# Performance work log

Hardware: AMD Instinct MI355X
Metric: run time of the kernel (lower is better)

Reference implementation:

```python
import jax, jax.numpy as jnp
import numpy as np

B, T, FEAT, IN = 32, 96, 2048, 4096  # batch, frames, feature_len, inshape (cat mode)


def setup_inputs() -> dict:
    key = jax.random.key(0)
    ks = jax.random.split(key, 12)
    s = 1.0 / np.sqrt(FEAT)  # PyTorch LSTMCell/Linear init scale ~ U(-1/sqrt(hidden), ...)
    f32 = jnp.float32
    return {
        "feature": jax.random.normal(ks[0], (B, T, IN), f32),
        "gumbel_u": jax.random.uniform(ks[1], (T - 1, B, 2), f32),
        "W_ih": jax.random.normal(ks[2], (4 * FEAT, IN), f32) * s,
        "b_ih": jax.random.normal(ks[3], (4 * FEAT,), f32) * s,
        "W_hh": jax.random.normal(ks[4], (4 * FEAT, FEAT), f32) * s,
        "b_hh": jax.random.normal(ks[5], (4 * FEAT,), f32) * s,
        "W_pred": jax.random.normal(ks[6], (2, FEAT), f32) * s,
        "b_pred": jax.random.normal(ks[7], (2,), f32) * s,
        "W_util": jax.random.normal(ks[8], (1, FEAT), f32) * s,
        "b_util": jax.random.normal(ks[9], (1,), f32) * s,
        "W_use": jax.random.normal(ks[10], (2, FEAT), f32) * s,
        "b_use": jax.random.normal(ks[11], (2,), f32) * s,
    }


def reference(feature, gumbel_u, W_ih, b_ih, W_hh, b_hh,
              W_pred, b_pred, W_util, b_util, W_use, b_use):
    tau = 1.0
    eps = 1e-10
    x = jnp.transpose(feature, (1, 0, 2))          # [T, B, IN]
    gnoise = -jnp.log(-jnp.log(gumbel_u + eps) + eps)  # Gumbel(0,1), [T-1, B, 2]

    def lstm_cell(x_t, h, c):
        gates = x_t @ W_ih.T + b_ih + h @ W_hh.T + b_hh  # [B, 4F]
        i, f, g, o = jnp.split(gates, 4, axis=-1)        # PyTorch gate order i,f,g,o
        c2 = jax.nn.sigmoid(f) * c + jax.nn.sigmoid(i) * jnp.tanh(g)
        h2 = jax.nn.sigmoid(o) * jnp.tanh(c2)
        return h2, c2

    def heads(h):
        return h @ W_pred.T + b_pred, h @ W_util.T + b_util

    h0 = jnp.zeros((x.shape[1], FEAT), x.dtype)
    h, c = lstm_cell(x[0], h0, h0)                   # step 0: no gating
    pred0, util0 = heads(h)

    def step(carry, inp):
        h_prev, c_prev = carry
        x_t, g_t = inp
        h_new, c2 = lstm_cell(x_t, h_prev, c_prev)
        logits = h_new @ W_use.T + b_use             # [B, 2]
        use = jax.nn.softmax((logits + g_t) / tau, axis=-1)  # soft gumbel-softmax
        # bmm(stack([h_prev, h_new], -1), use) == convex mix of the two states
        h2 = h_prev * use[:, :1] + h_new * use[:, 1:2]
        pred, util = heads(h2)
        return (h2, c2), (pred, util)

    _, (preds, utils) = jax.lax.scan(step, (h, c), (x[1:], gnoise))
    pred = jnp.concatenate([pred0[None], preds], axis=0)   # [T, B, 2]
    util = jnp.concatenate([util0[None], utils], axis=0)   # [T, B, 1]
    return pred, util
```

## Files before the change

kernel.cpp:

```cpp
#include <hip/hip_runtime.h>
#include <cstdint>
#include <cstddef>

#define TT 96
#define BB 32
#define FEATD 2048
#define IND 4096
#define NG 8192
#define MROWS 3072

typedef _Float16 half8 __attribute__((ext_vector_type(8)));
typedef _Float16 half4 __attribute__((ext_vector_type(4)));
typedef float f32x4 __attribute__((ext_vector_type(4)));

#define WS_FEAT16 0u
#define WS_HBUF   0u
#define WS_WIH16  25165824u
#define WS_WHH16  92274688u
#define WS_PRE16  125829120u
#define WS_GAB    176160768u
#define WS_HD     176185344u
#define WS_BAR    176222208u

#define NWG 256
#define BAR_WORDS (33 * 64)

__global__ void __launch_bounds__(256) k_convert(
    const float* __restrict__ feat, const float* __restrict__ wih,
    const float* __restrict__ whh,
    _Float16* __restrict__ feat16, _Float16* __restrict__ wih16,
    _Float16* __restrict__ whh16, unsigned* __restrict__ barr)
{
  size_t id = (size_t)blockIdx.x * blockDim.x + threadIdx.x;
  size_t stride = (size_t)gridDim.x * blockDim.x;
  for (size_t i = id; i < (size_t)MROWS * IND / 4; i += stride) {
    f32x4 v = ((const f32x4*)feat)[i];
    half4 h = { (_Float16)v[0], (_Float16)v[1], (_Float16)v[2], (_Float16)v[3] };
    ((half4*)feat16)[i] = h;
  }
  for (size_t i = id; i < (size_t)NG * IND / 4; i += stride) {
    f32x4 v = ((const f32x4*)wih)[i];
    half4 h = { (_Float16)v[0], (_Float16)v[1], (_Float16)v[2], (_Float16)v[3] };
    ((half4*)wih16)[i] = h;
  }
  for (size_t i = id; i < (size_t)NG * FEATD / 4; i += stride) {
    f32x4 v = ((const f32x4*)whh)[i];
    half4 h = { (_Float16)v[0], (_Float16)v[1], (_Float16)v[2], (_Float16)v[3] };
    ((half4*)whh16)[i] = h;
  }
  for (size_t i = id; i < BAR_WORDS; i += stride) barr[i] = 0u;
}

__device__ __forceinline__ void gload16(const _Float16* g, _Float16* l) {
  __builtin_amdgcn_global_load_lds(
      (const __attribute__((address_space(1))) void*)g,
      (__attribute__((address_space(3))) void*)l, 16, 0, 0);
}

__global__ void __launch_bounds__(256, 1) k_gemm(
    const _Float16* __restrict__ A,
    const _Float16* __restrict__ Bw,
    const float* __restrict__ bih, const float* __restrict__ bhh,
    _Float16* __restrict__ C)
{
  __shared__ __align__(16) _Float16 As[128 * 32];
  __shared__ __align__(16) _Float16 Bs[128 * 32];
  const int tid = threadIdx.x;
  const int lane = tid & 63;
  const int wave = tid >> 6;
  const int wm = wave >> 1, wn = wave & 1;
  const int mbase = blockIdx.y * 128;
  const int nbase = blockIdx.x * 128;

  f32x4 acc[4][4] = {};
  const int r0 = lane >> 2;
  const int kc = (lane & 3) * 8;
  const int rr = lane & 15;
  const int ko = (lane >> 4) * 8;

  for (int k0 = 0; k0 < IND; k0 += 32) {
    for (int i = 0; i < 2; ++i) {
      int seg = wave * 2 + i;
      int row = seg * 16 + r0;
      gload16(A + (size_t)(mbase + row) * IND + k0 + kc, As + seg * 512);
      gload16(Bw + (size_t)(nbase + row) * IND + k0 + kc, Bs + seg * 512);
    }
    __syncthreads();
    half8 af[4], bf[4];
    for (int f = 0; f < 4; ++f) {
      af[f] = *(const half8*)(As + (wm * 64 + f * 16 + rr) * 32 + ko);
      bf[f] = *(const half8*)(Bs + (wn * 64 + f * 16 + rr) * 32 + ko);
    }
    for (int fm = 0; fm < 4; ++fm)
      for (int fn = 0; fn < 4; ++fn)
        acc[fm][fn] = __builtin_amdgcn_mfma_f32_16x16x32_f16(af[fm], bf[fn], acc[fm][fn], 0, 0, 0);
    __syncthreads();
  }
  for (int fn = 0; fn < 4; ++fn) {
    int n = nbase + wn * 64 + fn * 16 + (lane & 15);
    float bias = bih[n] + bhh[n];
    for (int fm = 0; fm < 4; ++fm) {
      int m0 = mbase + wm * 64 + fm * 16 + (lane >> 4) * 4;
      for (int r = 0; r < 4; ++r)
        C[(size_t)(m0 + r) * NG + n] = (_Float16)(acc[fm][fn][r] + bias);
    }
  }
}

#define LDS_WHH 0
#define LDS_RED 131072
#define RED_STRIDE_F 1152
#define LDS_G   149504
#define LDS_C   153728
#define LDS_TOTAL 154752

__global__ void __launch_bounds__(512, 1) k_recur(
    const float* __restrict__ gumbel,
    const float* __restrict__ Wuse, const float* __restrict__ buse,
    const _Float16* __restrict__ whh16,
    const _Float16* __restrict__ pre16,
    _Float16* __restrict__ hbuf,
    float* __restrict__ gab,
    unsigned* __restrict__ barr)
{
  extern __shared__ __align__(16) char smem[];
  const int tid = threadIdx.x;
  const int wg = blockIdx.x;
  const int wave = tid >> 6, lane = tid & 63;
  float* Gf  = (float*)(smem + LDS_G);
  float* Cf  = (float*)(smem + LDS_C);
  float* RED = (float*)(smem + LDS_RED);

  {
    int c = tid >> 4;
    int grow = (c >> 3) * FEATD + wg * 8 + (c & 7);
    const _Float16* src = whh16 + (size_t)grow * FEATD;
    char* dst = smem + LDS_WHH + c * 4096;
    int x = c & 7;
    for (int i = 0; i < 16; ++i) {
      int g = (tid & 15) + i * 16;
      *(half8*)(dst + ((g ^ x) << 4)) = *(const half8*)(src + g * 8);
    }
  }
  for (int i = tid; i < 32 * 33; i += 512) Gf[i] = 0.f;
  for (int i = tid; i < 32 * 8;  i += 512) Cf[i] = 0.f;

  const int rr = lane & 15;
  const int lk = (lane >> 4) * 8;
  half8 uq0[8], uq1[8];
#pragma unroll
  for (int s = 0; s < 8; ++s) {
    int kk = wave * 256 + s * 32 + lk;
#pragma unroll
    for (int e = 0; e < 8; ++e) {
      uq0[s][e] = (_Float16)Wuse[kk + e];
      uq1[s][e] = (_Float16)Wuse[FEATD + kk + e];
    }
  }

  const int b_ = tid >> 3, fi_ = tid & 7;
  const float bq0 = buse[0], bq1 = buse[1];

  const _Float16* prbase = pre16 + ((size_t)b_ * TT) * NG + wg * 8 + fi_;
  _Float16 pf0 = 0, pf1 = 0, pf2 = 0, pf3 = 0;
  float gum0 = 0.f, gum1 = 0.f;
  if (tid < 256) {
    pf0 = prbase[0]; pf1 = prbase[FEATD]; pf2 = prbase[2 * FEATD]; pf3 = prbase[3 * FEATD];
  }
  __syncthreads();

  for (int t = 0; t < TT; ++t) {
    if (tid < 256) {
      float g0 = (float)pf0 + Gf[b_ * 33 + fi_];
      float g1 = (float)pf1 + Gf[b_ * 33 + fi_ + 8];
      float g2 = (float)pf2 + Gf[b_ * 33 + fi_ + 16];
      float g3 = (float)pf3 + Gf[b_ * 33 + fi_ + 24];
      float ig = 1.f / (1.f + __expf(-g0));
      float fg = 1.f / (1.f + __expf(-g1));
      float gg = tanhf(g2);
      float og = 1.f / (1.f + __expf(-g3));
      float cc = fg * Cf[b_ * 8 + fi_] + ig * gg;
      Cf[b_ * 8 + fi_] = cc;
      float hn = og * tanhf(cc);
      float hn_o = __shfl_xor(hn, 1);
      if ((fi_ & 1) == 0) {
        union { _Float16 h[2]; unsigned u; } pk;
        pk.h[0] = (_Float16)hn; pk.h[1] = (_Float16)hn_o;
        unsigned* dst = (unsigned*)(hbuf + (size_t)t * (BB * FEATD) + b_ * FEATD + wg * 8 + fi_);
        __hip_atomic_store(dst, pk.u, __ATOMIC_RELAXED, __HIP_MEMORY_SCOPE_AGENT);
      }
    }
    __syncthreads();
    if (tid == 0) {
      const unsigned tgt = (unsigned)(t + 1);
      const int g = wg >> 4;
      __hip_atomic_fetch_add(&barr[g * 64], 1u, __ATOMIC_RELAXED, __HIP_MEMORY_SCOPE_AGENT);
      if ((wg & 15) == 0) {
        while (__hip_atomic_load(&barr[g * 64], __ATOMIC_RELAXED, __HIP_MEMORY_SCOPE_AGENT) < 16u * tgt)
          __builtin_amdgcn_s_sleep(1);
        __hip_atomic_fetch_add(&barr[16 * 64], 1u, __ATOMIC_RELAXED, __HIP_MEMORY_SCOPE_AGENT);
        while (__hip_atomic_load(&barr[16 * 64], __ATOMIC_RELAXED, __HIP_MEMORY_SCOPE_AGENT) < 16u * tgt)
          __builtin_amdgcn_s_sleep(1);
        __hip_atomic_store(&barr[(17 + g) * 64], tgt, __ATOMIC_RELAXED, __HIP_MEMORY_SCOPE_AGENT);
      } else {
        while (__hip_atomic_load(&barr[(17 + g) * 64], __ATOMIC_RELAXED, __HIP_MEMORY_SCOPE_AGENT) < tgt)
          __builtin_amdgcn_s_sleep(1);
      }
    }
    __syncthreads();

    const _Float16* hb = hbuf + (size_t)t * (BB * FEATD);
    f32x4 acc[2][2] = {};
    float q0a = 0.f, q1a = 0.f, q0b = 0.f, q1b = 0.f;
    {
      const int c0 = rr, c1 = 16 + rr;
      const char* wsl = smem + LDS_WHH;
#pragma unroll
      for (int s = 0; s < 8; ++s) {
        int kk = wave * 256 + s * 32 + lk;
        half8 a0 = *(const half8*)(hb + rr * FEATD + kk);
        half8 a1 = *(const half8*)(hb + (16 + rr) * FEATD + kk);
        int g = kk >> 3;
        half8 b0 = *(const half8*)(wsl + c0 * 4096 + ((g ^ (c0 & 7)) << 4));
        half8 b1 = *(const half8*)(wsl + c1 * 4096 + ((g ^ (c1 & 7)) << 4));
        acc[0][0] = __builtin_amdgcn_mfma_f32_16x16x32_f16(a0, b0, acc[0][0], 0, 0, 0);
        acc[0][1] = __builtin_amdgcn_mfma_f32_16x16x32_f16(a0, b1, acc[0][1], 0, 0, 0);
        acc[1][0] = __builtin_amdgcn_mfma_f32_16x16x32_f16(a1, b0, acc[1][0], 0, 0, 0);
        acc[1][1] = __builtin_amdgcn_mfma_f32_16x16x32_f16(a1, b1, acc[1][1], 0, 0, 0);
#pragma unroll
        for (int e = 0; e < 8; ++e) {
          float xa = (float)a0[e], xb = (float)a1[e];
          q0a += xa * (float)uq0[s][e]; q1a += xa * (float)uq1[s][e];
          q0b += xb * (float)uq0[s][e]; q1b += xb * (float)uq1[s][e];
        }
      }
    }
    q0a += __shfl_xor(q0a, 16); q0a += __shfl_xor(q0a, 32);
    q1a += __shfl_xor(q1a, 16); q1a += __shfl_xor(q1a, 32);
    q0b += __shfl_xor(q0b, 16); q0b += __shfl_xor(q0b, 32);
    q1b += __shfl_xor(q1b, 16); q1b += __shfl_xor(q1b, 32);
    if (lane < 16) {
      float* pads = RED + (wave & 3) * RED_STRIDE_F + 32 + (wave >> 2) * 2;
      pads[rr * 36 + 0] = q0a; pads[rr * 36 + 1] = q1a;
      pads[(16 + rr) * 36 + 0] = q0b; pads[(16 + rr) * 36 + 1] = q1b;
    }
    {
      const int bb0 = (lane >> 4) * 4;
      const int cc0 = lane & 15;
      if (wave >= 4) {
        float* s0 = RED + (wave - 4) * RED_STRIDE_F;
        for (int fm = 0; fm < 2; ++fm)
          for (int fn = 0; fn < 2; ++fn)
            *(f32x4*)(s0 + (fn * 16 + cc0) * 36 + fm * 16 + bb0) = acc[fm][fn];
      }
      __syncthreads();
      if (wave < 4) {
        float* s0 = RED + wave * RED_STRIDE_F;
        for (int fm = 0; fm < 2; ++fm)
          for (int fn = 0; fn < 2; ++fn)
            acc[fm][fn] += *(f32x4*)(s0 + (fn * 16 + cc0) * 36 + fm * 16 + bb0);
        if (wave >= 2)
          for (int fm = 0; fm < 2; ++fm)
            for (int fn = 0; fn < 2; ++fn)
              *(f32x4*)(s0 + (fn * 16 + cc0) * 36 + fm * 16 + bb0) = acc[fm][fn];
      }
      __syncthreads();
      if (wave < 2) {
        float* s2 = RED + (wave + 2) * RED_STRIDE_F;
        for (int fm = 0; fm < 2; ++fm)
          for (int fn = 0; fn < 2; ++fn)
            acc[fm][fn] += *(f32x4*)(s2 + (fn * 16 + cc0) * 36 + fm * 16 + bb0);
        if (wave == 1) {
          float* s3 = RED + 3 * RED_STRIDE_F;
          for (int fm = 0; fm < 2; ++fm)
            for (int fn = 0; fn < 2; ++fn)
              *(f32x4*)(s3 + (fn * 16 + cc0) * 36 + fm * 16 + bb0) = acc[fm][fn];
        }
      }
      __syncthreads();
      if (wave == 0) {
        float* s3 = RED + 3 * RED_STRIDE_F;
        for (int fm = 0; fm < 2; ++fm)
          for (int fn = 0; fn < 2; ++fn) {
            acc[fm][fn] += *(f32x4*)(s3 + (fn * 16 + cc0) * 36 + fm * 16 + bb0);
            *(f32x4*)(RED + (fn * 16 + cc0) * 36 + fm * 16 + bb0) = acc[fm][fn];
          }
      }
      __syncthreads();
    }
    if (tid < 256) {
      float ga = 0.f, gb = 1.f;
      if (t > 0) {
        float q0 = bq0, q1 = bq1;
#pragma unroll
        for (int s2 = 0; s2 < 4; ++s2) {
          const float* pp = RED + s2 * RED_STRIDE_F + b_ * 36 + 32;
          q0 += pp[0] + pp[2]; q1 += pp[1] + pp[3];
        }
        float n0 = -logf(-logf(gum0 + 1e-10f) + 1e-10f);
        float n1 = -logf(-logf(gum1 + 1e-10f) + 1e-10f);
        float l0 = q0 + n0;
        float l1 = q1 + n1;
        float mx = fmaxf(l0, l1);
        float e0 = __expf(l0 - mx), e1 = __expf(l1 - mx);
        float inv = 1.f / (e0 + e1);
        ga = e0 * inv; gb = e1 * inv;
        if (wg == 0 && fi_ == 0) {
          gab[(t * BB + b_) * 2 + 0] = ga;
          gab[(t * BB + b_) * 2 + 1] = gb;
        }
      }
#pragma unroll
      for (int j = 0; j < 4; ++j) {
        int c = fi_ + 8 * j;
        Gf[b_ * 33 + c] = ga * Gf[b_ * 33 + c] + gb * RED[c * 36 + b_];
      }
      if (t + 1 < TT) {
        const _Float16* p = prbase + (size_t)(t + 1) * NG;
        pf0 = p[0]; pf1 = p[FEATD]; pf2 = p[2 * FEATD]; pf3 = p[3 * FEATD];
        gum0 = gumbel[(size_t)t * 64 + b_ * 2 + 0];
        gum1 = gumbel[(size_t)t * 64 + b_ * 2 + 1];
      }
    }
  }
}

__global__ void __launch_bounds__(256) k_heads(
    const _Float16* __restrict__ hbuf,
    const float* __restrict__ Wpred, const float* __restrict__ Wutil,
    float* __restrict__ hd)
{
  const int t = blockIdx.x;
  const int tid = threadIdx.x;
  const int b = tid >> 3, fi = tid & 7;
  const _Float16* h = hbuf + ((size_t)t * BB + b) * FEATD;
  float d0 = 0.f, d1 = 0.f, d2 = 0.f;
  for (int j = 0; j < 32; ++j) {
    int k = fi * 8 + j * 64;
    half8 v = *(const half8*)(h + k);
#pragma unroll
    for (int e = 0; e < 8; ++e) {
      float x = (float)v[e];
      d0 += x * Wpred[k + e];
      d1 += x * Wpred[FEATD + k + e];
      d2 += x * Wutil[k + e];
    }
  }
  for (int m = 1; m < 8; m <<= 1) {
    d0 += __shfl_xor(d0, m); d1 += __shfl_xor(d1, m); d2 += __shfl_xor(d2, m);
  }
  if (fi == 0) {
    float* o = hd + ((size_t)t * BB + b) * 3;
    o[0] = d0; o[1] = d1; o[2] = d2;
  }
}

__global__ void __launch_bounds__(64) k_scan(
    const float* __restrict__ hd,
    const float* __restrict__ gab,
    const float* __restrict__ bpred, const float* __restrict__ butil,
    float* __restrict__ out)
{
  const int b = threadIdx.x;
  if (b >= BB) return;
  const float bp0 = bpred[0], bp1 = bpred[1], bu0 = butil[0];
  float L0 = hd[b * 3 + 0], L1 = hd[b * 3 + 1], L2 = hd[b * 3 + 2];
  out[b * 2 + 0] = L0 + bp0;
  out[b * 2 + 1] = L1 + bp1;
  out[TT * BB * 2 + b] = L2 + bu0;
  for (int t = 1; t < TT; ++t) {
    float ga = gab[(t * BB + b) * 2 + 0];
    float gb = gab[(t * BB + b) * 2 + 1];
    const float* d = hd + ((size_t)t * BB + b) * 3;
    L0 = ga * L0 + gb * d[0];
    L1 = ga * L1 + gb * d[1];
    L2 = ga * L2 + gb * d[2];
    out[(t * BB + b) * 2 + 0] = L0 + bp0;
    out[(t * BB + b) * 2 + 1] = L1 + bp1;
    out[TT * BB * 2 + t * BB + b] = L2 + bu0;
  }
}

extern "C" void kernel_launch(void* const* d_in, const int* in_sizes, int n_in,
                              void* d_out, int out_size, void* d_ws, size_t ws_size,
                              hipStream_t stream) {
  const float* feat  = (const float*)d_in[0];
  const float* gumb  = (const float*)d_in[1];
  const float* Wih   = (const float*)d_in[2];
  const float* bih   = (const float*)d_in[3];
  const float* Whh   = (const float*)d_in[4];
  const float* bhh   = (const float*)d_in[5];
  const float* Wpred = (const float*)d_in[6];
  const float* bpred = (const float*)d_in[7];
  const float* Wutil = (const float*)d_in[8];
  const float* butil = (const float*)d_in[9];
  const float* Wuse  = (const float*)d_in[10];
  const float* buse  = (const float*)d_in[11];

  char* ws = (char*)d_ws;
  _Float16* feat16 = (_Float16*)(ws + WS_FEAT16);
  _Float16* hbufp  = (_Float16*)(ws + WS_HBUF);
  _Float16* wih16  = (_Float16*)(ws + WS_WIH16);
  _Float16* whh16  = (_Float16*)(ws + WS_WHH16);
  _Float16* pre16  = (_Float16*)(ws + WS_PRE16);
  float*    gabp   = (float*)(ws + WS_GAB);
  float*    hdp    = (float*)(ws + WS_HD);
  unsigned* barp   = (unsigned*)(ws + WS_BAR);

  (void)in_sizes; (void)n_in; (void)out_size; (void)ws_size;

  hipFuncSetAttribute((const void*)k_recur,
                      hipFuncAttributeMaxDynamicSharedMemorySize, LDS_TOTAL);

  k_convert<<<2048, 256, 0, stream>>>(feat, Wih, Whh, feat16, wih16, whh16, barp);
  dim3 g2(NG / 128, MROWS / 128);
  k_gemm<<<g2, 256, 0, stream>>>(feat16, wih16, bih, bhh, pre16);
  k_recur<<<NWG, 512, LDS_TOTAL, stream>>>(gumb, Wuse, buse, whh16, pre16,
                                           hbufp, gabp, barp);
  k_heads<<<TT, 256, 0, stream>>>(hbufp, Wpred, Wutil, hdp);
  k_scan<<<1, 64, 0, stream>>>(hdp, gabp, bpred, butil, (float*)d_out);
}
```

Before: 1.158 ms.

## Replace hierarchical grid barrier with flag-array barrier and streamline recurrent step

Replaces the two-level atomic counter barrier in the persistent recurrent kernel with a per-workgroup flag array that one wave polls in full, cutting barrier latency on every time step. It also keeps gate and cell state in registers instead of LDS and collapses the tree reduction to one sync. The next step's pre-activations and Gumbel values are now loaded before the MFMA phase, and the use-head dot products use fdot2. Risks include heavier polling traffic on the flag array and slightly different tanh and dot-product numerics.

```diff
diff --git a/kernel.cpp b/kernel.cpp
--- a/kernel.cpp
+++ b/kernel.cpp
@@ -11,6 +11,7 @@
 
 typedef _Float16 half8 __attribute__((ext_vector_type(8)));
 typedef _Float16 half4 __attribute__((ext_vector_type(4)));
+typedef _Float16 half2v __attribute__((ext_vector_type(2)));
 typedef float f32x4 __attribute__((ext_vector_type(4)));
 
 #define WS_FEAT16 0u
@@ -23,13 +24,12 @@
 #define WS_BAR    176222208u
 
 #define NWG 256
-#define BAR_WORDS (33 * 64)
 
 __global__ void __launch_bounds__(256) k_convert(
     const float* __restrict__ feat, const float* __restrict__ wih,
     const float* __restrict__ whh,
     _Float16* __restrict__ feat16, _Float16* __restrict__ wih16,
-    _Float16* __restrict__ whh16, unsigned* __restrict__ barr)
+    _Float16* __restrict__ whh16, unsigned* __restrict__ flags)
 {
   size_t id = (size_t)blockIdx.x * blockDim.x + threadIdx.x;
   size_t stride = (size_t)gridDim.x * blockDim.x;
@@ -48,7 +48,7 @@
     half4 h = { (_Float16)v[0], (_Float16)v[1], (_Float16)v[2], (_Float16)v[3] };
     ((half4*)whh16)[i] = h;
   }
-  for (size_t i = id; i < BAR_WORDS; i += stride) barr[i] = 0u;
+  if (id < NWG) flags[id] = 0u;
 }
 
 __device__ __forceinline__ void gload16(const _Float16* g, _Float16* l) {
@@ -110,9 +110,14 @@
 #define LDS_WHH 0
 #define LDS_RED 131072
 #define RED_STRIDE_F 1152
-#define LDS_G   149504
-#define LDS_C   153728
-#define LDS_TOTAL 154752
+#define LDS_TOTAL 149504
+
+__device__ __forceinline__ float fast_sigmoid(float x) {
+  return 1.f / (1.f + __expf(-x));
+}
+__device__ __forceinline__ float fast_tanh(float x) {
+  return 1.f - 2.f / (__expf(2.f * x) + 1.f);
+}
 
 __global__ void __launch_bounds__(512, 1) k_recur(
     const float* __restrict__ gumbel,
@@ -121,14 +126,12 @@
     const _Float16* __restrict__ pre16,
     _Float16* __restrict__ hbuf,
     float* __restrict__ gab,
-    unsigned* __restrict__ barr)
+    unsigned* __restrict__ flags)
 {
   extern __shared__ __align__(16) char smem[];
   const int tid = threadIdx.x;
   const int wg = blockIdx.x;
   const int wave = tid >> 6, lane = tid & 63;
-  float* Gf  = (float*)(smem + LDS_G);
-  float* Cf  = (float*)(smem + LDS_C);
   float* RED = (float*)(smem + LDS_RED);
 
   {
@@ -142,8 +145,6 @@
       *(half8*)(dst + ((g ^ x) << 4)) = *(const half8*)(src + g * 8);
     }
   }
-  for (int i = tid; i < 32 * 33; i += 512) Gf[i] = 0.f;
-  for (int i = tid; i < 32 * 8;  i += 512) Cf[i] = 0.f;
 
   const int rr = lane & 15;
   const int lk = (lane >> 4) * 8;
@@ -161,9 +162,11 @@
   const int b_ = tid >> 3, fi_ = tid & 7;
   const float bq0 = buse[0], bq1 = buse[1];
 
+  float G0 = 0.f, G1 = 0.f, G2 = 0.f, G3 = 0.f, cc = 0.f;
   const _Float16* prbase = pre16 + ((size_t)b_ * TT) * NG + wg * 8 + fi_;
   _Float16 pf0 = 0, pf1 = 0, pf2 = 0, pf3 = 0;
-  float gum0 = 0.f, gum1 = 0.f;
+  _Float16 pn0 = 0, pn1 = 0, pn2 = 0, pn3 = 0;
+  float gmc0 = 0.f, gmc1 = 0.f, gmn0 = 0.f, gmn1 = 0.f;
   if (tid < 256) {
     pf0 = prbase[0]; pf1 = prbase[FEATD]; pf2 = prbase[2 * FEATD]; pf3 = prbase[3 * FEATD];
   }
@@ -171,17 +174,12 @@
 
   for (int t = 0; t < TT; ++t) {
     if (tid < 256) {
-      float g0 = (float)pf0 + Gf[b_ * 33 + fi_];
-      float g1 = (float)pf1 + Gf[b_ * 33 + fi_ + 8];
-      float g2 = (float)pf2 + Gf[b_ * 33 + fi_ + 16];
-      float g3 = (float)pf3 + Gf[b_ * 33 + fi_ + 24];
-      float ig = 1.f / (1.f + __expf(-g0));
-      float fg = 1.f / (1.f + __expf(-g1));
-      float gg = tanhf(g2);
-      float og = 1.f / (1.f + __expf(-g3));
-      float cc = fg * Cf[b_ * 8 + fi_] + ig * gg;
-      Cf[b_ * 8 + fi_] = cc;
-      float hn = og * tanhf(cc);
+      float ig = fast_sigmoid((float)pf0 + G0);
+      float fg = fast_sigmoid((float)pf1 + G1);
+      float gg = fast_tanh((float)pf2 + G2);
+      float og = fast_sigmoid((float)pf3 + G3);
+      cc = fg * cc + ig * gg;
+      float hn = og * fast_tanh(cc);
       float hn_o = __shfl_xor(hn, 1);
       if ((fi_ & 1) == 0) {
         union { _Float16 h[2]; unsigned u; } pk;
@@ -191,23 +189,30 @@
       }
     }
     __syncthreads();
-    if (tid == 0) {
-      const unsigned tgt = (unsigned)(t + 1);
-      const int g = wg >> 4;
-      __hip_atomic_fetch_add(&barr[g * 64], 1u, __ATOMIC_RELAXED, __HIP_MEMORY_SCOPE_AGENT);
-      if ((wg & 15) == 0) {
-        while (__hip_atomic_load(&barr[g * 64], __ATOMIC_RELAXED, __HIP_MEMORY_SCOPE_AGENT) < 16u * tgt)
-          __builtin_amdgcn_s_sleep(1);
-        __hip_atomic_fetch_add(&barr[16 * 64], 1u, __ATOMIC_RELAXED, __HIP_MEMORY_SCOPE_AGENT);
-        while (__hip_atomic_load(&barr[16 * 64], __ATOMIC_RELAXED, __HIP_MEMORY_SCOPE_AGENT) < 16u * tgt)
-          __builtin_amdgcn_s_sleep(1);
-        __hip_atomic_store(&barr[(17 + g) * 64], tgt, __ATOMIC_RELAXED, __HIP_MEMORY_SCOPE_AGENT);
-      } else {
-        while (__hip_atomic_load(&barr[(17 + g) * 64], __ATOMIC_RELAXED, __HIP_MEMORY_SCOPE_AGENT) < tgt)
-          __builtin_amdgcn_s_sleep(1);
+    const unsigned tgt = (unsigned)(t + 1);
+    if (wave == 0) {
+      if (lane == 0)
+        __hip_atomic_store(&flags[wg], tgt, __ATOMIC_RELAXED, __HIP_MEMORY_SCOPE_AGENT);
+      for (;;) {
+        bool ok = true;
+#pragma unroll
+        for (int j = 0; j < 4; ++j) {
+          unsigned v = __hip_atomic_load(&flags[lane + j * 64],
+                                         __ATOMIC_RELAXED, __HIP_MEMORY_SCOPE_AGENT);
+          ok &= (v >= tgt);
+        }
+        if (__all(ok)) break;
+        __builtin_amdgcn_s_sleep(1);
       }
     }
     __syncthreads();
+
+    if (tid < 256 && t + 1 < TT) {
+      const _Float16* p = prbase + (size_t)(t + 1) * NG;
+      pn0 = p[0]; pn1 = p[FEATD]; pn2 = p[2 * FEATD]; pn3 = p[3 * FEATD];
+      gmn0 = gumbel[(size_t)t * 64 + b_ * 2 + 0];
+      gmn1 = gumbel[(size_t)t * 64 + b_ * 2 + 1];
+    }
 
     const _Float16* hb = hbuf + (size_t)t * (BB * FEATD);
     f32x4 acc[2][2] = {};
@@ -227,11 +232,16 @@
         acc[0][1] = __builtin_amdgcn_mfma_f32_16x16x32_f16(a0, b1, acc[0][1], 0, 0, 0);
         acc[1][0] = __builtin_amdgcn_mfma_f32_16x16x32_f16(a1, b0, acc[1][0], 0, 0, 0);
         acc[1][1] = __builtin_amdgcn_mfma_f32_16x16x32_f16(a1, b1, acc[1][1], 0, 0, 0);
-#pragma unroll
-        for (int e = 0; e < 8; ++e) {
-          float xa = (float)a0[e], xb = (float)a1[e];
-          q0a += xa * (float)uq0[s][e]; q1a += xa * (float)uq1[s][e];
-          q0b += xb * (float)uq0[s][e]; q1b += xb * (float)uq1[s][e];
+        const half2v* a0p = (const half2v*)&a0;
+        const half2v* a1p = (const half2v*)&a1;
+        const half2v* u0p = (const half2v*)&uq0[s];
+        const half2v* u1p = (const half2v*)&uq1[s];
+#pragma unroll
+        for (int e = 0; e < 4; ++e) {
+          q0a = __builtin_amdgcn_fdot2(a0p[e], u0p[e], q0a, false);
+          q1a = __builtin_amdgcn_fdot2(a0p[e], u1p[e], q1a, false);
+          q0b = __builtin_amdgcn_fdot2(a1p[e], u0p[e], q0b, false);
+          q1b = __builtin_amdgcn_fdot2(a1p[e], u1p[e], q1b, false);
         }
       }
     }
@@ -257,33 +267,9 @@
       if (wave < 4) {
         float* s0 = RED + wave * RED_STRIDE_F;
         for (int fm = 0; fm < 2; ++fm)
-          for (int fn = 0; fn < 2; ++fn)
+          for (int fn = 0; fn < 2; ++fn) {
             acc[fm][fn] += *(f32x4*)(s0 + (fn * 16 + cc0) * 36 + fm * 16 + bb0);
-        if (wave >= 2)
-          for (int fm = 0; fm < 2; ++fm)
-            for (int fn = 0; fn < 2; ++fn)
-              *(f32x4*)(s0 + (fn * 16 + cc0) * 36 + fm * 16 + bb0) = acc[fm][fn];
-      }
-      __syncthreads();
-      if (wave < 2) {
-        float* s2 = RED + (wave + 2) * RED_STRIDE_F;
-        for (int fm = 0; fm < 2; ++fm)
-          for (int fn = 0; fn < 2; ++fn)
-            acc[fm][fn] += *(f32x4*)(s2 + (fn * 16 + cc0) * 36 + fm * 16 + bb0);
-        if (wave == 1) {
-          float* s3 = RED + 3 * RED_STRIDE_F;
-          for (int fm = 0; fm < 2; ++fm)
-            for (int fn = 0; fn < 2; ++fn)
-              *(f32x4*)(s3 + (fn * 16 + cc0) * 36 + fm * 16 + bb0) = acc[fm][fn];
-        }
-      }
-      __syncthreads();
-      if (wave == 0) {
-        float* s3 = RED + 3 * RED_STRIDE_F;
-        for (int fm = 0; fm < 2; ++fm)
-          for (int fn = 0; fn < 2; ++fn) {
-            acc[fm][fn] += *(f32x4*)(s3 + (fn * 16 + cc0) * 36 + fm * 16 + bb0);
-            *(f32x4*)(RED + (fn * 16 + cc0) * 36 + fm * 16 + bb0) = acc[fm][fn];
+            *(f32x4*)(s0 + (fn * 16 + cc0) * 36 + fm * 16 + bb0) = acc[fm][fn];
           }
       }
       __syncthreads();
@@ -297,8 +283,8 @@
           const float* pp = RED + s2 * RED_STRIDE_F + b_ * 36 + 32;
           q0 += pp[0] + pp[2]; q1 += pp[1] + pp[3];
         }
-        float n0 = -logf(-logf(gum0 + 1e-10f) + 1e-10f);
-        float n1 = -logf(-logf(gum1 + 1e-10f) + 1e-10f);
+        float n0 = -logf(-logf(gmc0 + 1e-10f) + 1e-10f);
+        float n1 = -logf(-logf(gmc1 + 1e-10f) + 1e-10f);
         float l0 = q0 + n0;
         float l1 = q1 + n1;
         float mx = fmaxf(l0, l1);
@@ -310,17 +296,19 @@
           gab[(t * BB + b_) * 2 + 1] = gb;
         }
       }
-#pragma unroll
-      for (int j = 0; j < 4; ++j) {
-        int c = fi_ + 8 * j;
-        Gf[b_ * 33 + c] = ga * Gf[b_ * 33 + c] + gb * RED[c * 36 + b_];
-      }
-      if (t + 1 < TT) {
-        const _Float16* p = prbase + (size_t)(t + 1) * NG;
-        pf0 = p[0]; pf1 = p[FEATD]; pf2 = p[2 * FEATD]; pf3 = p[3 * FEATD];
-        gum0 = gumbel[(size_t)t * 64 + b_ * 2 + 0];
-        gum1 = gumbel[(size_t)t * 64 + b_ * 2 + 1];
-      }
+      {
+        const int base = fi_ * 36 + b_;
+        float m0 = RED[base] + RED[RED_STRIDE_F + base] + RED[2 * RED_STRIDE_F + base] + RED[3 * RED_STRIDE_F + base];
+        float m1 = RED[base + 8 * 36] + RED[RED_STRIDE_F + base + 8 * 36] + RED[2 * RED_STRIDE_F + base + 8 * 36] + RED[3 * RED_STRIDE_F + base + 8 * 36];
+        float m2 = RED[base + 16 * 36] + RED[RED_STRIDE_F + base + 16 * 36] + RED[2 * RED_STRIDE_F + base + 16 * 36] + RED[3 * RED_STRIDE_F + base + 16 * 36];
+        float m3 = RED[base + 24 * 36] + RED[RED_STRIDE_F + base + 24 * 36] + RED[2 * RED_STRIDE_F + base + 24 * 36] + RED[3 * RED_STRIDE_F + base + 24 * 36];
+        G0 = ga * G0 + gb * m0;
+        G1 = ga * G1 + gb * m1;
+        G2 = ga * G2 + gb * m2;
+        G3 = ga * G3 + gb * m3;
+      }
+      pf0 = pn0; pf1 = pn1; pf2 = pn2; pf3 = pn3;
+      gmc0 = gmn0; gmc1 = gmn1;
     }
   }
 }
@@ -405,18 +393,18 @@
   _Float16* pre16  = (_Float16*)(ws + WS_PRE16);
   float*    gabp   = (float*)(ws + WS_GAB);
   float*    hdp    = (float*)(ws + WS_HD);
-  unsigned* barp   = (unsigned*)(ws + WS_BAR);
+  unsigned* flagp  = (unsigned*)(ws + WS_BAR);
 
   (void)in_sizes; (void)n_in; (void)out_size; (void)ws_size;
 
   hipFuncSetAttribute((const void*)k_recur,
                       hipFuncAttributeMaxDynamicSharedMemorySize, LDS_TOTAL);
 
-  k_convert<<<2048, 256, 0, stream>>>(feat, Wih, Whh, feat16, wih16, whh16, barp);
+  k_convert<<<2048, 256, 0, stream>>>(feat, Wih, Whh, feat16, wih16, whh16, flagp);
   dim3 g2(NG / 128, MROWS / 128);
   k_gemm<<<g2, 256, 0, stream>>>(feat16, wih16, bih, bhh, pre16);
   k_recur<<<NWG, 512, LDS_TOTAL, stream>>>(gumb, Wuse, buse, whh16, pre16,
-                                           hbufp, gabp, barp);
+                                           hbufp, gabp, flagp);
   k_heads<<<TT, 256, 0, stream>>>(hbufp, Wpred, Wutil, hdp);
   k_scan<<<1, 64, 0, stream>>>(hdp, gabp, bpred, butil, (float*)d_out);
 }
```

New measurement: 1.323 ms. 14.2% more time.
